# Kernel tuning notes

Hardware: AMD Instinct MI355X
Metric: run time of the kernel (lower is better)

Reference implementation:

```python
import jax, jax.numpy as jnp
import numpy as np

K = 10
ALPHA = 0.1

def setup_inputs() -> dict:
    key = jax.random.key(0)
    k1, k2, k3, k4 = jax.random.split(key, 4)
    N, E, IN, HID, OUT = 100000, 3200000, 512, 256, 64
    x = jax.random.normal(k1, (N, IN), dtype=jnp.float32)
    edge_index = jax.random.randint(k2, (2, E), 0, N, dtype=jnp.int64)
    W1 = jax.random.normal(k3, (IN, HID), dtype=jnp.float32) * (1.0 / np.sqrt(IN))
    b1 = jnp.zeros((HID,), jnp.float32)
    W2 = jax.random.normal(k4, (HID, OUT), dtype=jnp.float32) * (1.0 / np.sqrt(HID))
    b2 = jnp.zeros((OUT,), jnp.float32)
    return {"x": x, "edge_index": edge_index, "W1": W1, "b1": b1, "W2": W2, "b2": b2}

def reference(x, edge_index, W1, b1, W2, b2):
    N = x.shape[0]
    # gcn_norm with self-loops (PyG default for APPNP)
    loop = jnp.arange(N, dtype=edge_index.dtype)
    src = jnp.concatenate([edge_index[0], loop])  # [E+N]
    dst = jnp.concatenate([edge_index[1], loop])
    ones = jnp.ones(src.shape[0], dtype=x.dtype)
    deg = jax.ops.segment_sum(ones, dst, num_segments=N)
    dis = jnp.where(deg > 0, jax.lax.rsqrt(deg), 0.0)
    norm = dis[src] * dis[dst]  # [E+N]

    # 2-layer MLP (dropout disabled: eval mode)
    h = jnp.maximum(x @ W1 + b1, 0.0) @ W2 + b2  # [N, out]

    # K-step PPR diffusion: z <- alpha*h + (1-alpha)*A_hat z
    def step(z, _):
        agg = jax.ops.segment_sum(norm[:, None] * z[src], dst, num_segments=N)
        return ALPHA * h + (1.0 - ALPHA) * agg, None

    z, _ = jax.lax.scan(step, h, None, length=K)
    return jax.nn.log_softmax(z, axis=-1)
```

## Files before the change

kernel.cpp:

```cpp
#include <hip/hip_runtime.h>
#include <hip/hip_bf16.h>

#define ALPHA_F 0.1f
#define KSTEPS 10
#define BKT_SH 9
#define P1_CHUNK 8192

typedef __attribute__((ext_vector_type(8))) short bf16x8;
typedef __attribute__((ext_vector_type(4))) float f32x4;

__device__ __forceinline__ unsigned short f2bf(float f) {
  union { float f; unsigned int u; } v; v.f = f;
  unsigned int u = v.u;
  u += 0x7FFFu + ((u >> 16) & 1u);
  return (unsigned short)(u >> 16);
}
__device__ __forceinline__ float bflo(unsigned int u) { return __uint_as_float(u << 16); }
__device__ __forceinline__ float bfhi(unsigned int u) { return __uint_as_float(u & 0xFFFF0000u); }


__global__ __launch_bounds__(256)
void p0_hist(const int* __restrict__ dstv, int E, int* __restrict__ bhist) {
  __shared__ int h[256];
  int t = threadIdx.x;
  h[t] = 0;
  __syncthreads();
  int b0 = blockIdx.x * P1_CHUNK;
  int lim = min(P1_CHUNK, E - b0);
  for (int i = t; i < lim; i += 256) atomicAdd(&h[dstv[b0 + i] >> BKT_SH], 1);
  __syncthreads();
  if (h[t]) atomicAdd(&bhist[t], h[t]);
}

__global__ void p0_scan(const int* __restrict__ bhist, int* __restrict__ bbase,
                        int* __restrict__ gcur, int* __restrict__ rowptr, int N, int E) {
  __shared__ int s[256];
  int t = threadIdx.x;
  int mine = bhist[t];
  s[t] = mine;
  __syncthreads();
  for (int off = 1; off < 256; off <<= 1) {
    int v = (t >= off) ? s[t - off] : 0;
    __syncthreads();
    s[t] += v;
    __syncthreads();
  }
  int excl = s[t] - mine;
  bbase[t] = excl;
  gcur[t] = excl;
  if (t == 0) rowptr[N] = E;
}

__global__ __launch_bounds__(256)
void p1_scatter(const int* __restrict__ srcv, const int* __restrict__ dstv, int E,
                int* __restrict__ gcur, int2* __restrict__ tmp) {
  __shared__ int h[256];
  __shared__ int loc[256];
  int t = threadIdx.x;
  int b0 = blockIdx.x * P1_CHUNK;
  int lim = min(P1_CHUNK, E - b0);
  h[t] = 0;
  __syncthreads();
  for (int i = t; i < lim; i += 256) atomicAdd(&h[dstv[b0 + i] >> BKT_SH], 1);
  __syncthreads();
  loc[t] = h[t] ? atomicAdd(&gcur[t], h[t]) : 0;
  __syncthreads();
  h[t] = 0;
  __syncthreads();
  for (int i = t; i < lim; i += 256) {
    int d = dstv[b0 + i], s = srcv[b0 + i];
    int b = d >> BKT_SH;
    int pos = loc[b] + atomicAdd(&h[b], 1);
    tmp[pos] = make_int2(s, d);
  }
}

__global__ __launch_bounds__(256)
void p2_bucket(const int2* __restrict__ tmp, const int* __restrict__ bbase,
               const int* __restrict__ bhist, int* __restrict__ counts,
               int* __restrict__ rowptr, int2* __restrict__ out, int N) {
  __shared__ int h1[512];
  __shared__ int cur[512];
  __shared__ int s2[256];
  const int t = threadIdx.x;
  const int b = blockIdx.x;
  const int base = bbase[b];
  const int sz = bhist[b];
  const int r0 = b << BKT_SH;
  const int nrows = min(512, N - r0);

  h1[t] = 0; h1[t + 256] = 0;
  __syncthreads();
  for (int i = t; i < sz; i += 256) atomicAdd(&h1[tmp[base + i].y - r0], 1);
  __syncthreads();
  if (t < nrows) counts[r0 + t] = h1[t];
  if (t + 256 < nrows) counts[r0 + t + 256] = h1[t + 256];
  int a = h1[2 * t], c = h1[2 * t + 1];
  s2[t] = a + c;
  __syncthreads();
  for (int off = 1; off < 256; off <<= 1) {
    int v = (t >= off) ? s2[t - off] : 0;
    __syncthreads();
    s2[t] += v;
    __syncthreads();
  }
  int excl2 = s2[t] - (a + c);
  cur[2 * t] = excl2;
  cur[2 * t + 1] = excl2 + a;
  __syncthreads();
  if (t < nrows) rowptr[r0 + t] = base + cur[t];
  if (t + 256 < nrows) rowptr[r0 + t + 256] = base + cur[t + 256];
  __syncthreads();
  for (int i = t; i < sz; i += 256) {
    int2 e = tmp[base + i];
    int p = base + atomicAdd(&cur[e.y - r0], 1);
    out[p] = e;
  }
}

__global__ void k_dis(const int* __restrict__ counts, float* __restrict__ dis, int N) {
  int i = blockIdx.x * 256 + threadIdx.x;
  if (i < N) dis[i] = rsqrtf((float)(counts[i] + 1));
}

__global__ void p3_weights(int2* __restrict__ edges, const float* __restrict__ dis, int E) {
  int i = blockIdx.x * 256 + threadIdx.x;
  if (i >= E) return;
  int2 e = edges[i];
  edges[i] = make_int2(e.x, __float_as_int(dis[e.x] * dis[e.y]));
}

__global__ void k_wconv(const float* __restrict__ W, unsigned short* __restrict__ WT,
                        int Kd, int Nd) {
  int idx = blockIdx.x * 256 + threadIdx.x;
  if (idx >= Kd * Nd) return;
  int n = idx / Kd, k = idx % Kd;
  WT[idx] = f2bf(W[(size_t)k * Nd + n]);
}

template<int BN, int WR, int WC, bool CONVERT_A, bool RELU, bool OUT_BF16>
__global__ __launch_bounds__(256)
void gemm_kernel(const void* __restrict__ Ag_, const unsigned short* __restrict__ BT,
                 const float* __restrict__ bias, void* __restrict__ out_,
                 int M, int Kd) {
  constexpr int MF = 64 / (16 * WR);
  constexpr int NF = BN / (16 * WC);
  __shared__ __align__(16) unsigned short As[64][40];
  __shared__ __align__(16) unsigned short Bs[BN][40];
  const int t = threadIdx.x;
  const int m0 = blockIdx.x * 64;
  const int lane = t & 63;
  const int w = t >> 6;
  const int wr = w / WC, wc = w % WC;
  const int lrow = t >> 2;
  const int lcb = t & 3;

  f32x4 acc[MF][NF] = {};

  for (int k0 = 0; k0 < Kd; k0 += 32) {
    {
      int gm = m0 + lrow;
      uint4 tv;
      unsigned short* tmp = (unsigned short*)&tv;
      if (CONVERT_A) {
        const float* A = (const float*)Ag_;
        if (gm < M) {
          const float* p = A + (size_t)gm * Kd + k0 + lcb * 8;
          float4 va = *(const float4*)p;
          float4 vb = *(const float4*)(p + 4);
          tmp[0] = f2bf(va.x); tmp[1] = f2bf(va.y); tmp[2] = f2bf(va.z); tmp[3] = f2bf(va.w);
          tmp[4] = f2bf(vb.x); tmp[5] = f2bf(vb.y); tmp[6] = f2bf(vb.z); tmp[7] = f2bf(vb.w);
        } else {
          tv = uint4{0, 0, 0, 0};
        }
      } else {
        const unsigned short* A = (const unsigned short*)Ag_;
        if (gm < M) tv = *(const uint4*)(A + (size_t)gm * Kd + k0 + lcb * 8);
        else        tv = uint4{0, 0, 0, 0};
      }
      *(uint4*)&As[lrow][lcb * 8] = tv;
    }
#pragma unroll
    for (int i = 0; i < BN / 64; ++i) {
      int ch = t + 256 * i;
      int row = ch >> 2, kc = (ch & 3) * 8;
      *(uint4*)&Bs[row][kc] = *(const uint4*)(BT + (size_t)row * Kd + k0 + kc);
    }
    __syncthreads();

    bf16x8 af[MF], bfv[NF];
#pragma unroll
    for (int mi = 0; mi < MF; ++mi)
      af[mi] = *(const bf16x8*)&As[wr * MF * 16 + mi * 16 + (lane & 15)][(lane >> 4) * 8];
#pragma unroll
    for (int ni = 0; ni < NF; ++ni)
      bfv[ni] = *(const bf16x8*)&Bs[wc * NF * 16 + ni * 16 + (lane & 15)][(lane >> 4) * 8];
#pragma unroll
    for (int mi = 0; mi < MF; ++mi)
#pragma unroll
      for (int ni = 0; ni < NF; ++ni)
        acc[mi][ni] = __builtin_amdgcn_mfma_f32_16x16x32_bf16(af[mi], bfv[ni], acc[mi][ni], 0, 0, 0);
    __syncthreads();
  }

  float* outf = (float*)out_;
  unsigned short* outb = (unsigned short*)out_;
#pragma unroll
  for (int mi = 0; mi < MF; ++mi) {
#pragma unroll
    for (int ni = 0; ni < NF; ++ni) {
      int gn = wc * NF * 16 + ni * 16 + (lane & 15);
      float bv = bias[gn];
#pragma unroll
      for (int j = 0; j < 4; ++j) {
        int gm = m0 + wr * MF * 16 + mi * 16 + (lane >> 4) * 4 + j;
        if (gm < M) {
          float v = acc[mi][ni][j] + bv;
          if (RELU) v = fmaxf(v, 0.f);
          if (OUT_BF16) outb[(size_t)gm * BN + gn] = f2bf(v);
          else          outf[(size_t)gm * BN + gn] = v;
        }
      }
    }
  }
}

template<bool FINAL>
__global__ __launch_bounds__(256)
void prop_kernel(const unsigned short* __restrict__ zin,
                 const unsigned short* __restrict__ hb,
                 void* __restrict__ zout, const int* __restrict__ rowptr,
                 const int2* __restrict__ edges, const float* __restrict__ dis, int N) {
  int wid = (blockIdx.x * 256 + threadIdx.x) >> 6;
  wid = __builtin_amdgcn_readfirstlane(wid);
  if (wid >= N) return;
  const int lane = threadIdx.x & 63;
  const int g  = lane >> 3;
  const int lg = lane & 7;
  const int r = wid;

  float acc[8] = {0.f, 0.f, 0.f, 0.f, 0.f, 0.f, 0.f, 0.f};
  const int start = rowptr[r], end = rowptr[r + 1];
  for (int e = start; e < end; e += 64) {
    int na = end - e; if (na > 64) na = 64;
    int2 ed = make_int2(0, 0);
    if (lane < na) ed = edges[e + lane];
#pragma unroll 4
    for (int j = 0; j < na; j += 8) {
      int jj = j + g;
      int cj = __shfl(ed.x, jj);
      float wj = __shfl(__int_as_float(ed.y), jj);
      uint4 zr = *(const uint4*)(zin + (size_t)cj * 64 + 8 * lg);
      acc[0] += wj * bflo(zr.x); acc[1] += wj * bfhi(zr.x);
      acc[2] += wj * bflo(zr.y); acc[3] += wj * bfhi(zr.y);
      acc[4] += wj * bflo(zr.z); acc[5] += wj * bfhi(zr.z);
      acc[6] += wj * bflo(zr.w); acc[7] += wj * bfhi(zr.w);
    }
  }
#pragma unroll
  for (int k = 0; k < 8; ++k) {
    acc[k] += __shfl_xor(acc[k], 8);
    acc[k] += __shfl_xor(acc[k], 16);
    acc[k] += __shfl_xor(acc[k], 32);
  }

  float dr = dis[r];
  float sw = dr * dr;
  uint4 zs = *(const uint4*)(zin + (size_t)r * 64 + 8 * lg);
  uint4 hr = *(const uint4*)(hb + (size_t)r * 64 + 8 * lg);
  float selfz[8] = { bflo(zs.x), bfhi(zs.x), bflo(zs.y), bfhi(zs.y),
                     bflo(zs.z), bfhi(zs.z), bflo(zs.w), bfhi(zs.w) };
  float hv[8]    = { bflo(hr.x), bfhi(hr.x), bflo(hr.y), bfhi(hr.y),
                     bflo(hr.z), bfhi(hr.z), bflo(hr.w), bfhi(hr.w) };
  float f[8];
#pragma unroll
  for (int k = 0; k < 8; ++k)
    f[k] = ALPHA_F * hv[k] + (1.f - ALPHA_F) * (acc[k] + sw * selfz[k]);

  if (!FINAL) {
    if (g == 0) {
      uint4 o;
      o.x = (unsigned)f2bf(f[0]) | ((unsigned)f2bf(f[1]) << 16);
      o.y = (unsigned)f2bf(f[2]) | ((unsigned)f2bf(f[3]) << 16);
      o.z = (unsigned)f2bf(f[4]) | ((unsigned)f2bf(f[5]) << 16);
      o.w = (unsigned)f2bf(f[6]) | ((unsigned)f2bf(f[7]) << 16);
      *(uint4*)((unsigned short*)zout + (size_t)r * 64 + 8 * lg) = o;
    }
  } else {
    float m = f[0];
#pragma unroll
    for (int k = 1; k < 8; ++k) m = fmaxf(m, f[k]);
    m = fmaxf(m, __shfl_xor(m, 1));
    m = fmaxf(m, __shfl_xor(m, 2));
    m = fmaxf(m, __shfl_xor(m, 4));
    float s = 0.f;
#pragma unroll
    for (int k = 0; k < 8; ++k) s += __expf(f[k] - m);
    s += __shfl_xor(s, 1);
    s += __shfl_xor(s, 2);
    s += __shfl_xor(s, 4);
    float ls = __logf(s);
    if (g == 0) {
      float* op = (float*)zout + (size_t)r * 64 + 8 * lg;
      *(float4*)op       = make_float4(f[0] - m - ls, f[1] - m - ls, f[2] - m - ls, f[3] - m - ls);
      *(float4*)(op + 4) = make_float4(f[4] - m - ls, f[5] - m - ls, f[6] - m - ls, f[7] - m - ls);
    }
  }
}

extern "C" void kernel_launch(void* const* d_in, const int* in_sizes, int n_in,
                              void* d_out, int out_size, void* d_ws, size_t ws_size,
                              hipStream_t stream) {
  const float* x  = (const float*)d_in[0];
  const int*   ei = (const int*)d_in[1];
  const float* W1 = (const float*)d_in[2];
  const float* b1 = (const float*)d_in[3];
  const float* W2 = (const float*)d_in[4];
  const float* b2 = (const float*)d_in[5];

  const int IN = 512, HID = 256, OUT = 64;
  const int N = in_sizes[0] / IN;
  const int E = in_sizes[1] / 2;
  const int* srcv = ei;
  const int* dstv = ei + E;
  const int NBUCK = (N + (1 << BKT_SH) - 1) >> BKT_SH;

  char* p = (char*)d_ws;
  auto alloc = [&](size_t bytes) -> void* {
    void* r = (void*)p;
    p += (bytes + 255) & ~(size_t)255;
    return r;
  };
  int*   bhist  = (int*)alloc(256 * 4);
  int*   bbase  = (int*)alloc(256 * 4);
  int*   gcur   = (int*)alloc(256 * 4);
  int*   counts = (int*)alloc((size_t)N * 4);
  float* dis    = (float*)alloc((size_t)N * 4);
  int*   rowptr = (int*)alloc((size_t)(N + 1) * 4);
  int2*  edges  = (int2*)alloc((size_t)E * 8);
  unsigned short* WT1 = (unsigned short*)alloc((size_t)IN * HID * 2);
  unsigned short* WT2 = (unsigned short*)alloc((size_t)HID * OUT * 2);
  unsigned short* hidb = (unsigned short*)alloc((size_t)N * HID * 2);
  unsigned short* hb   = (unsigned short*)alloc((size_t)N * OUT * 2);
  int2* tmp = (int2*)hidb;
  unsigned short* zA = hidb;
  unsigned short* zB = hidb + (size_t)N * OUT;

  hipMemsetAsync(bhist, 0, 256 * 4, stream);

  const int p1blocks = (E + P1_CHUNK - 1) / P1_CHUNK;
  p0_hist<<<p1blocks, 256, 0, stream>>>(dstv, E, bhist);
  p0_scan<<<1, 256, 0, stream>>>(bhist, bbase, gcur, rowptr, N, E);
  p1_scatter<<<p1blocks, 256, 0, stream>>>(srcv, dstv, E, gcur, tmp);
  p2_bucket<<<NBUCK, 256, 0, stream>>>(tmp, bbase, bhist, counts, rowptr, edges, N);
  k_dis<<<(N + 255) / 256, 256, 0, stream>>>(counts, dis, N);
  p3_weights<<<(E + 255) / 256, 256, 0, stream>>>(edges, dis, E);

  k_wconv<<<(IN * HID + 255) / 256, 256, 0, stream>>>(W1, WT1, IN, HID);
  k_wconv<<<(HID * OUT + 255) / 256, 256, 0, stream>>>(W2, WT2, HID, OUT);

  const int gblocks = (N + 63) / 64;
  gemm_kernel<256, 1, 4, true, true, true><<<gblocks, 256, 0, stream>>>(
      x, WT1, b1, hidb, N, IN);
  gemm_kernel<64, 2, 2, false, false, true><<<gblocks, 256, 0, stream>>>(
      hidb, WT2, b2, hb, N, HID);

  const int pblocks = (N + 3) / 4;
  const unsigned short* zcur = hb;
  for (int it = 0; it < KSTEPS - 1; ++it) {
    unsigned short* znext = (it & 1) ? zB : zA;
    prop_kernel<false><<<pblocks, 256, 0, stream>>>(zcur, hb, znext, rowptr, edges, dis, N);
    zcur = znext;
  }
  prop_kernel<true><<<pblocks, 256, 0, stream>>>(zcur, hb, d_out, rowptr, edges, dis, N);
}
```

Baseline: 833.6 us.

## Rewrite MLP GEMMs with MFMA-fragment-tiled layouts and direct global-to-LDS loads

Replaces the generic templated GEMM with two specialised kernels that use 128-row tiles, a 64-wide K step, and weights and hidden activations pre-permuted into a fragment-contiguous tiled layout. The B tiles, and the A tiles in the second GEMM, are loaded with global_load_lds straight into LDS, skipping register staging. The first GEMM writes its hidden output in the tiled layout the second GEMM reads. This is meant to cut LDS bank conflicts, per-tile address math and sync overhead in the MLP stage, at the cost of hardcoded dimensions and a larger LDS footprint per block.

```diff
diff --git a/kernel.cpp b/kernel.cpp
--- a/kernel.cpp
+++ b/kernel.cpp
@@ -17,6 +17,12 @@
 }
 __device__ __forceinline__ float bflo(unsigned int u) { return __uint_as_float(u << 16); }
 __device__ __forceinline__ float bfhi(unsigned int u) { return __uint_as_float(u & 0xFFFF0000u); }
+
+__device__ __forceinline__ void gload16(const void* g, void* l) {
+  __builtin_amdgcn_global_load_lds(
+      (const __attribute__((address_space(1))) void*)g,
+      (__attribute__((address_space(3))) void*)l, 16, 0, 0);
+}
 
 
 __global__ __launch_bounds__(256)
@@ -130,96 +136,166 @@
   edges[i] = make_int2(e.x, __float_as_int(dis[e.x] * dis[e.y]));
 }
 
-__global__ void k_wconv(const float* __restrict__ W, unsigned short* __restrict__ WT,
-                        int Kd, int Nd) {
+
+__global__ void k_wconv1(const float* __restrict__ W, unsigned short* __restrict__ WT) {
   int idx = blockIdx.x * 256 + threadIdx.x;
-  if (idx >= Kd * Nd) return;
-  int n = idx / Kd, k = idx % Kd;
-  WT[idx] = f2bf(W[(size_t)k * Nd + n]);
-}
-
-template<int BN, int WR, int WC, bool CONVERT_A, bool RELU, bool OUT_BF16>
-__global__ __launch_bounds__(256)
-void gemm_kernel(const void* __restrict__ Ag_, const unsigned short* __restrict__ BT,
-                 const float* __restrict__ bias, void* __restrict__ out_,
-                 int M, int Kd) {
-  constexpr int MF = 64 / (16 * WR);
-  constexpr int NF = BN / (16 * WC);
-  __shared__ __align__(16) unsigned short As[64][40];
-  __shared__ __align__(16) unsigned short Bs[BN][40];
+  if (idx >= 512 * 256) return;
+  int e = idx & 7, n = (idx >> 3) & 15, q = (idx >> 7) & 7;
+  int nsub = (idx >> 10) & 15, kstep = idx >> 14;
+  int k = kstep * 64 + q * 8 + e;
+  int ncol = nsub * 16 + n;
+  WT[idx] = f2bf(W[(size_t)k * 256 + ncol]);
+}
+
+__global__ void k_wconv2(const float* __restrict__ W, unsigned short* __restrict__ WT) {
+  int idx = blockIdx.x * 256 + threadIdx.x;
+  if (idx >= 256 * 64) return;
+  int e = idx & 7, n = (idx >> 3) & 15, q = (idx >> 7) & 7;
+  int nsub = (idx >> 10) & 3, kstep = idx >> 12;
+  int k = kstep * 64 + q * 8 + e;
+  int ncol = nsub * 16 + n;
+  WT[idx] = f2bf(W[(size_t)k * 64 + ncol]);
+}
+
+__global__ __launch_bounds__(512)
+void gemm1_kernel(const float* __restrict__ X, const unsigned short* __restrict__ Bt,
+                  const float* __restrict__ bias, unsigned short* __restrict__ outT,
+                  int M) {
+  __shared__ __align__(16) unsigned short Al[8192];
+  __shared__ __align__(16) unsigned short Bl[16384];
   const int t = threadIdx.x;
-  const int m0 = blockIdx.x * 64;
+  const int m0 = blockIdx.x * 128;
   const int lane = t & 63;
   const int w = t >> 6;
-  const int wr = w / WC, wc = w % WC;
-  const int lrow = t >> 2;
-  const int lcb = t & 3;
-
-  f32x4 acc[MF][NF] = {};
-
-  for (int k0 = 0; k0 < Kd; k0 += 32) {
-    {
-      int gm = m0 + lrow;
-      uint4 tv;
-      unsigned short* tmp = (unsigned short*)&tv;
-      if (CONVERT_A) {
-        const float* A = (const float*)Ag_;
-        if (gm < M) {
-          const float* p = A + (size_t)gm * Kd + k0 + lcb * 8;
-          float4 va = *(const float4*)p;
-          float4 vb = *(const float4*)(p + 4);
-          tmp[0] = f2bf(va.x); tmp[1] = f2bf(va.y); tmp[2] = f2bf(va.z); tmp[3] = f2bf(va.w);
-          tmp[4] = f2bf(vb.x); tmp[5] = f2bf(vb.y); tmp[6] = f2bf(vb.z); tmp[7] = f2bf(vb.w);
-        } else {
-          tv = uint4{0, 0, 0, 0};
+  const int wm = w >> 2, wn = w & 3;
+
+  const int sm = ((t >> 7) << 4) + (t & 15);
+  const int sq = (t >> 4) & 7;
+  const int r1 = m0 + sm;
+  const int r2 = r1 + 64;
+  const bool g1 = r1 < M, g2 = r2 < M;
+
+  f32x4 acc[4][4] = {};
+
+  for (int ks = 0; ks < 8; ++ks) {
+    const int kc = ks * 64 + sq * 8;
+    uint4 v1 = {0, 0, 0, 0}, v2 = {0, 0, 0, 0};
+    if (g1) {
+      const float* p = X + (size_t)r1 * 512 + kc;
+      float4 a = *(const float4*)p, b = *(const float4*)(p + 4);
+      unsigned short* o = (unsigned short*)&v1;
+      o[0] = f2bf(a.x); o[1] = f2bf(a.y); o[2] = f2bf(a.z); o[3] = f2bf(a.w);
+      o[4] = f2bf(b.x); o[5] = f2bf(b.y); o[6] = f2bf(b.z); o[7] = f2bf(b.w);
+    }
+    if (g2) {
+      const float* p = X + (size_t)r2 * 512 + kc;
+      float4 a = *(const float4*)p, b = *(const float4*)(p + 4);
+      unsigned short* o = (unsigned short*)&v2;
+      o[0] = f2bf(a.x); o[1] = f2bf(a.y); o[2] = f2bf(a.z); o[3] = f2bf(a.w);
+      o[4] = f2bf(b.x); o[5] = f2bf(b.y); o[6] = f2bf(b.z); o[7] = f2bf(b.w);
+    }
+    *(uint4*)&Al[t * 8] = v1;
+    *(uint4*)&Al[(t + 512) * 8] = v2;
+
+    const unsigned short* bs = Bt + ks * 16384;
+    gload16(bs + (size_t)t * 8,          &Bl[t * 8]);
+    gload16(bs + (size_t)(t + 512) * 8,  &Bl[(t + 512) * 8]);
+    gload16(bs + (size_t)(t + 1024) * 8, &Bl[(t + 1024) * 8]);
+    gload16(bs + (size_t)(t + 1536) * 8, &Bl[(t + 1536) * 8]);
+    __syncthreads();
+
+#pragma unroll
+    for (int kk = 0; kk < 2; ++kk) {
+      bf16x8 af[4], bfv[4];
+#pragma unroll
+      for (int mi = 0; mi < 4; ++mi)
+        af[mi] = *(const bf16x8*)&Al[((wm * 4 + mi) * 128 + kk * 64 + (lane >> 4) * 16 + (lane & 15)) * 8];
+#pragma unroll
+      for (int ni = 0; ni < 4; ++ni)
+        bfv[ni] = *(const bf16x8*)&Bl[((wn * 4 + ni) * 128 + kk * 64 + (lane >> 4) * 16 + (lane & 15)) * 8];
+#pragma unroll
+      for (int mi = 0; mi < 4; ++mi)
+#pragma unroll
+        for (int ni = 0; ni < 4; ++ni)
+          acc[mi][ni] = __builtin_amdgcn_mfma_f32_16x16x32_bf16(af[mi], bfv[ni], acc[mi][ni], 0, 0, 0);
+    }
+    __syncthreads();
+  }
+
+  unsigned short* ob = outT + (size_t)blockIdx.x * 32768;
+#pragma unroll
+  for (int mi = 0; mi < 4; ++mi) {
+#pragma unroll
+    for (int ni = 0; ni < 4; ++ni) {
+      int n = wn * 64 + ni * 16 + (lane & 15);
+      float bv = bias[n];
+      int kstep = n >> 6, q = (n >> 3) & 7, e = n & 7;
+#pragma unroll
+      for (int j = 0; j < 4; ++j) {
+        int lm = wm * 64 + mi * 16 + (lane >> 4) * 4 + j;
+        if (m0 + lm < M) {
+          float v = fmaxf(acc[mi][ni][j] + bv, 0.f);
+          int msub = lm >> 4, mm = lm & 15;
+          ob[((((kstep * 8 + msub) * 8 + q) * 16 + mm) * 8) + e] = f2bf(v);
         }
-      } else {
-        const unsigned short* A = (const unsigned short*)Ag_;
-        if (gm < M) tv = *(const uint4*)(A + (size_t)gm * Kd + k0 + lcb * 8);
-        else        tv = uint4{0, 0, 0, 0};
       }
-      *(uint4*)&As[lrow][lcb * 8] = tv;
-    }
-#pragma unroll
-    for (int i = 0; i < BN / 64; ++i) {
-      int ch = t + 256 * i;
-      int row = ch >> 2, kc = (ch & 3) * 8;
-      *(uint4*)&Bs[row][kc] = *(const uint4*)(BT + (size_t)row * Kd + k0 + kc);
-    }
-    __syncthreads();
-
-    bf16x8 af[MF], bfv[NF];
-#pragma unroll
-    for (int mi = 0; mi < MF; ++mi)
-      af[mi] = *(const bf16x8*)&As[wr * MF * 16 + mi * 16 + (lane & 15)][(lane >> 4) * 8];
-#pragma unroll
-    for (int ni = 0; ni < NF; ++ni)
-      bfv[ni] = *(const bf16x8*)&Bs[wc * NF * 16 + ni * 16 + (lane & 15)][(lane >> 4) * 8];
-#pragma unroll
-    for (int mi = 0; mi < MF; ++mi)
-#pragma unroll
-      for (int ni = 0; ni < NF; ++ni)
-        acc[mi][ni] = __builtin_amdgcn_mfma_f32_16x16x32_bf16(af[mi], bfv[ni], acc[mi][ni], 0, 0, 0);
-    __syncthreads();
-  }
-
-  float* outf = (float*)out_;
-  unsigned short* outb = (unsigned short*)out_;
-#pragma unroll
-  for (int mi = 0; mi < MF; ++mi) {
-#pragma unroll
-    for (int ni = 0; ni < NF; ++ni) {
-      int gn = wc * NF * 16 + ni * 16 + (lane & 15);
+    }
+  }
+}
+
+__global__ __launch_bounds__(256)
+void gemm2_kernel(const unsigned short* __restrict__ At, const unsigned short* __restrict__ Bt,
+                  const float* __restrict__ bias, unsigned short* __restrict__ hb, int M) {
+  __shared__ __align__(16) unsigned short Al[8192];
+  __shared__ __align__(16) unsigned short Bl[4096];
+  const int t = threadIdx.x;
+  const int m0 = blockIdx.x * 128;
+  const int lane = t & 63;
+  const int w = t >> 6;
+  const int wm = w >> 1, wn = w & 1;
+
+  f32x4 acc[4][2] = {};
+
+  const unsigned short* ab = At + (size_t)blockIdx.x * 32768;
+  for (int ks = 0; ks < 4; ++ks) {
+    const unsigned short* as = ab + ks * 8192;
+    gload16(as + (size_t)t * 8,         &Al[t * 8]);
+    gload16(as + (size_t)(t + 256) * 8, &Al[(t + 256) * 8]);
+    gload16(as + (size_t)(t + 512) * 8, &Al[(t + 512) * 8]);
+    gload16(as + (size_t)(t + 768) * 8, &Al[(t + 768) * 8]);
+    const unsigned short* bs = Bt + ks * 4096;
+    gload16(bs + (size_t)t * 8,         &Bl[t * 8]);
+    gload16(bs + (size_t)(t + 256) * 8, &Bl[(t + 256) * 8]);
+    __syncthreads();
+
+#pragma unroll
+    for (int kk = 0; kk < 2; ++kk) {
+      bf16x8 af[4], bfv[2];
+#pragma unroll
+      for (int mi = 0; mi < 4; ++mi)
+        af[mi] = *(const bf16x8*)&Al[((wm * 4 + mi) * 128 + kk * 64 + (lane >> 4) * 16 + (lane & 15)) * 8];
+#pragma unroll
+      for (int ni = 0; ni < 2; ++ni)
+        bfv[ni] = *(const bf16x8*)&Bl[((wn * 2 + ni) * 128 + kk * 64 + (lane >> 4) * 16 + (lane & 15)) * 8];
+#pragma unroll
+      for (int mi = 0; mi < 4; ++mi)
+#pragma unroll
+        for (int ni = 0; ni < 2; ++ni)
+          acc[mi][ni] = __builtin_amdgcn_mfma_f32_16x16x32_bf16(af[mi], bfv[ni], acc[mi][ni], 0, 0, 0);
+    }
+    __syncthreads();
+  }
+
+#pragma unroll
+  for (int mi = 0; mi < 4; ++mi) {
+#pragma unroll
+    for (int ni = 0; ni < 2; ++ni) {
+      int gn = wn * 32 + ni * 16 + (lane & 15);
       float bv = bias[gn];
 #pragma unroll
       for (int j = 0; j < 4; ++j) {
-        int gm = m0 + wr * MF * 16 + mi * 16 + (lane >> 4) * 4 + j;
-        if (gm < M) {
-          float v = acc[mi][ni][j] + bv;
-          if (RELU) v = fmaxf(v, 0.f);
-          if (OUT_BF16) outb[(size_t)gm * BN + gn] = f2bf(v);
-          else          outf[(size_t)gm * BN + gn] = v;
-        }
+        int gm = m0 + wm * 64 + mi * 16 + (lane >> 4) * 4 + j;
+        if (gm < M) hb[(size_t)gm * 64 + gn] = f2bf(acc[mi][ni][j] + bv);
       }
     }
   }
@@ -324,6 +400,7 @@
   const int* srcv = ei;
   const int* dstv = ei + E;
   const int NBUCK = (N + (1 << BKT_SH) - 1) >> BKT_SH;
+  const int MT = (N + 127) / 128;
 
   char* p = (char*)d_ws;
   auto alloc = [&](size_t bytes) -> void* {
@@ -338,13 +415,13 @@
   float* dis    = (float*)alloc((size_t)N * 4);
   int*   rowptr = (int*)alloc((size_t)(N + 1) * 4);
   int2*  edges  = (int2*)alloc((size_t)E * 8);
-  unsigned short* WT1 = (unsigned short*)alloc((size_t)IN * HID * 2);
-  unsigned short* WT2 = (unsigned short*)alloc((size_t)HID * OUT * 2);
-  unsigned short* hidb = (unsigned short*)alloc((size_t)N * HID * 2);
+  unsigned short* WT1t = (unsigned short*)alloc((size_t)IN * HID * 2);
+  unsigned short* WT2t = (unsigned short*)alloc((size_t)HID * OUT * 2);
+  unsigned short* hidT = (unsigned short*)alloc((size_t)MT * 32768 * 2);
   unsigned short* hb   = (unsigned short*)alloc((size_t)N * OUT * 2);
-  int2* tmp = (int2*)hidb;
-  unsigned short* zA = hidb;
-  unsigned short* zB = hidb + (size_t)N * OUT;
+  int2* tmp = (int2*)hidT;
+  unsigned short* zA = hidT;
+  unsigned short* zB = hidT + (size_t)N * OUT;
 
   hipMemsetAsync(bhist, 0, 256 * 4, stream);
 
@@ -356,14 +433,11 @@
   k_dis<<<(N + 255) / 256, 256, 0, stream>>>(counts, dis, N);
   p3_weights<<<(E + 255) / 256, 256, 0, stream>>>(edges, dis, E);
 
-  k_wconv<<<(IN * HID + 255) / 256, 256, 0, stream>>>(W1, WT1, IN, HID);
-  k_wconv<<<(HID * OUT + 255) / 256, 256, 0, stream>>>(W2, WT2, HID, OUT);
-
-  const int gblocks = (N + 63) / 64;
-  gemm_kernel<256, 1, 4, true, true, true><<<gblocks, 256, 0, stream>>>(
-      x, WT1, b1, hidb, N, IN);
-  gemm_kernel<64, 2, 2, false, false, true><<<gblocks, 256, 0, stream>>>(
-      hidb, WT2, b2, hb, N, HID);
+  k_wconv1<<<(IN * HID + 255) / 256, 256, 0, stream>>>(W1, WT1t);
+  k_wconv2<<<(HID * OUT + 255) / 256, 256, 0, stream>>>(W2, WT2t);
+
+  gemm1_kernel<<<MT, 512, 0, stream>>>(x, WT1t, b1, hidT, N);
+  gemm2_kernel<<<MT, 256, 0, stream>>>(hidT, WT2t, b2, hb, N);
 
   const int pblocks = (N + 3) / 4;
   const unsigned short* zcur = hb;
```

Result: no change. 820.2 us (-1.6%).
